# Performance work log

Hardware: AMD Instinct MI355X
Metric: run time of the kernel (lower is better)

Reference implementation:

```python
import jax, jax.numpy as jnp
import numpy as np

N_NODES = 50000
N_EDGES = 800000
IN_FEATS = 128
H_FEATS = 32
HEADS = 4
OUT_FEATS = 32
OUT_HEADS = 1
NEG_SLOPE = 0.2


def setup_inputs() -> dict:
    key = jax.random.key(0)
    ks = jax.random.split(key, 20)
    s = 0.05
    return {
        "features": jax.random.normal(ks[0], (N_NODES, IN_FEATS), jnp.float32),
        "src": jax.random.randint(ks[1], (N_EDGES,), 0, N_NODES, jnp.int32),
        "dst": jax.random.randint(ks[2], (N_EDGES,), 0, N_NODES, jnp.int32),
        "Ws0": jax.random.normal(ks[3], (IN_FEATS, HEADS * H_FEATS), jnp.float32) * s,
        "bs0": jnp.zeros((HEADS * H_FEATS,), jnp.float32),
        "Wd0": jax.random.normal(ks[4], (IN_FEATS, HEADS * H_FEATS), jnp.float32) * s,
        "bd0": jnp.zeros((HEADS * H_FEATS,), jnp.float32),
        "a0": jax.random.normal(ks[5], (HEADS, H_FEATS), jnp.float32) * s,
        "Ws1": jax.random.normal(ks[6], (HEADS * H_FEATS, HEADS * H_FEATS), jnp.float32) * s,
        "bs1": jnp.zeros((HEADS * H_FEATS,), jnp.float32),
        "Wd1": jax.random.normal(ks[7], (HEADS * H_FEATS, HEADS * H_FEATS), jnp.float32) * s,
        "bd1": jnp.zeros((HEADS * H_FEATS,), jnp.float32),
        "a1": jax.random.normal(ks[8], (HEADS, H_FEATS), jnp.float32) * s,
        "Ws2": jax.random.normal(ks[9], (HEADS * H_FEATS, OUT_HEADS * OUT_FEATS), jnp.float32) * s,
        "bs2": jnp.zeros((OUT_HEADS * OUT_FEATS,), jnp.float32),
        "Wd2": jax.random.normal(ks[10], (HEADS * H_FEATS, OUT_HEADS * OUT_FEATS), jnp.float32) * s,
        "bd2": jnp.zeros((OUT_HEADS * OUT_FEATS,), jnp.float32),
        "a2": jax.random.normal(ks[11], (OUT_HEADS, OUT_FEATS), jnp.float32) * s,
    }


def gatv2_conv(x, src, dst, Ws, bs, Wd, bd, attn, n_nodes):
    """DGL GATv2Conv (share_weights=False, residual=False, no dropout)."""
    heads, f = attn.shape
    feat_src = (x @ Ws + bs).reshape(-1, heads, f)  # [N, H, F]
    feat_dst = (x @ Wd + bd).reshape(-1, heads, f)  # [N, H, F]
    # per-edge GATv2 score: LeakyReLU(Wsrc h_u + Wdst h_v) . a
    e = jax.nn.leaky_relu(feat_src[src] + feat_dst[dst], NEG_SLOPE)  # [E, H, F]
    logits = jnp.einsum("ehf,hf->eh", e, attn)  # [E, H]
    # edge softmax over incoming edges of each dst node
    m = jax.ops.segment_max(logits, dst, num_segments=n_nodes)  # [N, H]
    ex = jnp.exp(logits - m[dst])
    denom = jax.ops.segment_sum(ex, dst, num_segments=n_nodes)  # [N, H]
    alpha = ex / denom[dst]  # [E, H]
    # scatter-aggregate messages
    msg = feat_src[src] * alpha[..., None]  # [E, H, F]
    return jax.ops.segment_sum(msg, dst, num_segments=n_nodes)  # [N, H, F]


def reference(features, src, dst,
              Ws0, bs0, Wd0, bd0, a0,
              Ws1, bs1, Wd1, bd1, a1,
              Ws2, bs2, Wd2, bd2, a2):
    n = features.shape[0]
    h = gatv2_conv(features, src, dst, Ws0, bs0, Wd0, bd0, a0, n)
    h = jax.nn.relu(h.reshape(n, -1))
    h = gatv2_conv(h, src, dst, Ws1, bs1, Wd1, bd1, a1, n)
    h = jax.nn.relu(h.reshape(n, -1))
    h = gatv2_conv(h, src, dst, Ws2, bs2, Wd2, bd2, a2, n)
    return h.mean(axis=1)  # [N, OUT_FEATS]
```

## Files before the change

kernel.cpp:

```cpp
#include <hip/hip_runtime.h>

typedef __attribute__((ext_vector_type(8))) short bf16x8;
typedef __attribute__((ext_vector_type(4))) float f32x4;

#define LOG2E 1.4426950408889634f

#define BINSH 8
#define NBIN 196
#define CHUNK 4096
#define K4CAP 6144

__device__ __forceinline__ unsigned bf_rn(float f) {
    unsigned u = __float_as_uint(f);
    u += 0x7fffu + ((u >> 16) & 1u);
    return u >> 16;
}
__device__ __forceinline__ float bf_lo(unsigned u) { return __uint_as_float(u << 16); }
__device__ __forceinline__ float bf_hi(unsigned u) { return __uint_as_float(u & 0xffff0000u); }

template <int CTRL>
__device__ __forceinline__ float dpp_radd(float x) {
    int t = __builtin_amdgcn_update_dpp(0, __float_as_int(x), CTRL, 0xF, 0xF, true);
    return x + __int_as_float(t);
}
__device__ __forceinline__ float sum8(float p) {
    p = dpp_radd<0x141>(p);
    p = dpp_radd<0x1B>(p);
    p = dpp_radd<0xB1>(p);
    return p;
}
__device__ __forceinline__ float sum4(float p) {
    p = dpp_radd<0xB1>(p);
    p = dpp_radd<0x4E>(p);
    return p;
}
__device__ __forceinline__ float dpp_swap1(float x) {
    return __int_as_float(__builtin_amdgcn_update_dpp(0, __float_as_int(x), 0xB1, 0xF, 0xF, true));
}

__device__ __forceinline__ float fast_exp2(float x) {
#if __has_builtin(__builtin_amdgcn_exp2f)
    return __builtin_amdgcn_exp2f(x);
#else
    return __expf(x * 0.6931471805599453f);
#endif
}


__global__ __launch_bounds__(256) void bin_count(const int* __restrict__ dst,
                                                 int* __restrict__ binCnt, int e) {
    __shared__ int hist[NBIN];
    for (int t = threadIdx.x; t < NBIN; t += 256) hist[t] = 0;
    __syncthreads();
    int base = blockIdx.x * CHUNK;
    int cnt = min(CHUNK, e - base);
    for (int j = threadIdx.x; j < cnt; j += 256)
        atomicAdd(&hist[dst[base + j] >> BINSH], 1);
    __syncthreads();
    for (int t = threadIdx.x; t < NBIN; t += 256)
        if (hist[t]) atomicAdd(&binCnt[t], hist[t]);
}

__global__ void bin_scan(const int* __restrict__ binCnt, int* __restrict__ binBase,
                         int* __restrict__ binCur, int* __restrict__ rowp, int n, int e) {
    int t = threadIdx.x;
    int v = (t < NBIN) ? binCnt[t] : 0;
    int lane = t & 63, w = t >> 6;
    int incl = v;
    for (int off = 1; off < 64; off <<= 1) {
        int tt = __shfl_up(incl, off);
        if (lane >= off) incl += tt;
    }
    __shared__ int wsum[4];
    if (lane == 63) wsum[w] = incl;
    __syncthreads();
    int wpre = 0;
    for (int i = 0; i < w; ++i) wpre += wsum[i];
    int excl = wpre + incl - v;
    if (t < NBIN) { binBase[t] = excl; binCur[t] = excl; }
    if (t == 0) { binBase[NBIN] = e; rowp[n] = e; }
}

__global__ __launch_bounds__(256) void bin_scatter(
    const int* __restrict__ src, const int* __restrict__ dst,
    int* __restrict__ binCur, unsigned* __restrict__ ebin, int e) {
    __shared__ int hist[256];
    __shared__ int seg[256];
    __shared__ int gbase[NBIN];
    __shared__ unsigned pack[CHUNK];
    for (int t = threadIdx.x; t < 256; t += 256) hist[t] = 0;
    __syncthreads();
    int base = blockIdx.x * CHUNK;
    int cnt = min(CHUNK, e - base);

    for (int j = threadIdx.x; j < cnt; j += 256)
        atomicAdd(&hist[dst[base + j] >> BINSH], 1);
    __syncthreads();
    if (threadIdx.x < 64) {
        int l = threadIdx.x;
        int s = 0, loc[4];
#pragma unroll
        for (int k = 0; k < 4; ++k) { loc[k] = s; s += hist[l * 4 + k]; }
        int incl = s;
        for (int off = 1; off < 64; off <<= 1) {
            int tt = __shfl_up(incl, off);
            if (l >= off) incl += tt;
        }
        int excl = incl - s;
#pragma unroll
        for (int k = 0; k < 4; ++k) seg[l * 4 + k] = excl + loc[k];
    }
    __syncthreads();
    if (threadIdx.x < NBIN && hist[threadIdx.x])
        gbase[threadIdx.x] = atomicAdd(&binCur[threadIdx.x], hist[threadIdx.x]);
    __syncthreads();
    for (int t = threadIdx.x; t < 256; t += 256) hist[t] = seg[t];
    __syncthreads();
    for (int j = threadIdx.x; j < cnt; j += 256) {
        int d = dst[base + j], s = src[base + j];
        int b = d >> BINSH, dl = d & ((1 << BINSH) - 1);
        int pos = atomicAdd(&hist[b], 1);
        pack[pos] = ((unsigned)b << 24) | ((unsigned)dl << 16) | (unsigned)s;
    }
    __syncthreads();
    for (int j = threadIdx.x; j < cnt; j += 256) {
        unsigned wv = pack[j];
        int b = wv >> 24;
        ebin[gbase[b] + (j - seg[b])] = wv;
    }
}

__global__ __launch_bounds__(256) void csr_build(
    const unsigned* __restrict__ ebin, const int* __restrict__ binBase,
    int* __restrict__ rowp, int* __restrict__ csrc, int n) {
    __shared__ int hist[256];
    __shared__ int seg[256];
    __shared__ unsigned stage[K4CAP];
    int b = blockIdx.x;
    int e0 = binBase[b], e1 = binBase[b + 1];
    int n0 = b << BINSH;
    int nn = min(256, n - n0);
    for (int t = threadIdx.x; t < 256; t += 256) hist[t] = 0;
    __syncthreads();
    for (int i = e0 + threadIdx.x; i < e1; i += 256) {
        unsigned wv = ebin[i];
        atomicAdd(&hist[(wv >> 16) & 255], 1);
        int off = i - e0;
        if (off < K4CAP) stage[off] = wv;
    }
    __syncthreads();
    if (threadIdx.x < 64) {
        int l = threadIdx.x;
        int s = 0, loc[4];
#pragma unroll
        for (int k = 0; k < 4; ++k) { loc[k] = s; s += hist[l * 4 + k]; }
        int incl = s;
        for (int off = 1; off < 64; off <<= 1) {
            int tt = __shfl_up(incl, off);
            if (l >= off) incl += tt;
        }
        int excl = incl - s;
#pragma unroll
        for (int k = 0; k < 4; ++k) seg[l * 4 + k] = excl + loc[k];
    }
    __syncthreads();
    for (int t = threadIdx.x; t < nn; t += 256) rowp[n0 + t] = e0 + seg[t];
    for (int t = threadIdx.x; t < 256; t += 256) hist[t] = seg[t];
    __syncthreads();
    for (int i = e0 + threadIdx.x; i < e1; i += 256) {
        int off = i - e0;
        unsigned wv = (off < K4CAP) ? stage[off] : ebin[i];
        int dl = (wv >> 16) & 255;
        int pos = e0 + atomicAdd(&hist[dl], 1);
        csrc[pos] = (int)(wv & 0xFFFFu);
    }
}


__global__ __launch_bounds__(256) void prep(
    const float* __restrict__ x, unsigned short* __restrict__ xb, int n4,
    const float* __restrict__ Ws0, const float* __restrict__ Wd0,
    const float* __restrict__ Ws1, const float* __restrict__ Wd1,
    const float* __restrict__ Ws2, const float* __restrict__ Wd2,
    unsigned short* __restrict__ wt0, unsigned short* __restrict__ wt1,
    unsigned short* __restrict__ wt2, int* __restrict__ binCnt) {
    int gid = blockIdx.x * blockDim.x + threadIdx.x;
    if (gid < NBIN) binCnt[gid] = 0;
    if (gid < n4) {
        float4 v = *(const float4*)(x + (size_t)gid * 4);
        ushort4 r;
        r.x = (unsigned short)bf_rn(v.x); r.y = (unsigned short)bf_rn(v.y);
        r.z = (unsigned short)bf_rn(v.z); r.w = (unsigned short)bf_rn(v.w);
        *(ushort4*)(xb + (size_t)gid * 4) = r;
    } else {
        int g = gid - n4;
        if (g < 65536) {
            int l = g >> 15, loc = g & 32767;
            int c = loc >> 7, k = loc & 127;
            const float* W = (c < 128) ? (l ? Ws1 : Ws0) : (l ? Wd1 : Wd0);
            int cc = c & 127;
            float v = W[(size_t)k * 128 + cc];
            (l ? wt1 : wt0)[loc] = (unsigned short)bf_rn(v);
        } else if (g < 65536 + 8192) {
            int loc = g - 65536;
            int c = loc >> 7, k = loc & 127;
            const float* W = (c < 32) ? Ws2 : Wd2;
            int cc = (c < 32) ? c : c - 32;
            float v = W[(size_t)k * 32 + cc];
            wt2[loc] = (unsigned short)bf_rn(v);
        }
    }
}


template <int COLS2>
__global__ __launch_bounds__(256) void gemm_dual2(
    const unsigned short* __restrict__ xb, const unsigned short* __restrict__ wt,
    const float* __restrict__ bs, const float* __restrict__ bd,
    unsigned short* __restrict__ fs, unsigned short* __restrict__ fd,
    int n, int nch) {
    constexpr int C  = COLS2 / 2;
    constexpr int NC = COLS2 / 64;

    const int lane = threadIdx.x & 63;
    const int m = lane & 15, quad = lane >> 4;
    const int gwid = blockIdx.x * 4 + (threadIdx.x >> 6);
    const int nwaves = gridDim.x * 4;
    const int cs = gwid % NC;
    const int cstride = nwaves / NC;

    float biasv[4];
#pragma unroll
    for (int ct = 0; ct < 4; ++ct) {
        int col = cs * 64 + ct * 16 + m;
        biasv[ct] = (col < C) ? bs[col] : bd[col - C];
    }

    for (int chunk = gwid / NC; chunk < nch; chunk += cstride) {
        const size_t r0 = (size_t)chunk * 64;

        f32x4 acc[4][4];
#pragma unroll
        for (int rt = 0; rt < 4; ++rt)
#pragma unroll
            for (int ct = 0; ct < 4; ++ct) acc[rt][ct] = (f32x4){0.f, 0.f, 0.f, 0.f};

#pragma unroll
        for (int ks = 0; ks < 4; ++ks) {
            const int ko = ks * 32 + quad * 8;
            bf16x8 a[4], b[4];
#pragma unroll
            for (int rt = 0; rt < 4; ++rt)
                a[rt] = *(const bf16x8*)(xb + (r0 + rt * 16 + m) * 128 + ko);
#pragma unroll
            for (int ct = 0; ct < 4; ++ct)
                b[ct] = *(const bf16x8*)(wt + (size_t)(cs * 64 + ct * 16 + m) * 128 + ko);
#pragma unroll
            for (int rt = 0; rt < 4; ++rt)
#pragma unroll
                for (int ct = 0; ct < 4; ++ct)
                    acc[rt][ct] = __builtin_amdgcn_mfma_f32_16x16x32_bf16(a[rt], b[ct], acc[rt][ct], 0, 0, 0);
        }

        const int odd = m & 1;
#pragma unroll
        for (int ct = 0; ct < 4; ++ct) {
            int colE = cs * 64 + ct * 16 + (m & ~1);
            unsigned short* ptr = (colE < C) ? fs : fd;
            int cc = (colE < C) ? colE : colE - C;
#pragma unroll
            for (int rt = 0; rt < 4; ++rt) {
                float v0 = acc[rt][ct][0] + biasv[ct];
                float v1 = acc[rt][ct][1] + biasv[ct];
                float v2 = acc[rt][ct][2] + biasv[ct];
                float v3 = acc[rt][ct][3] + biasv[ct];
                float s0 = dpp_swap1(v0), s1 = dpp_swap1(v1);
                float s2 = dpp_swap1(v2), s3 = dpp_swap1(v3);
                float aLo = odd ? s2 : v0, aHi = odd ? v2 : s0;
                float bLo = odd ? s3 : v1, bHi = odd ? v3 : s1;
                int rowA = (int)r0 + rt * 16 + quad * 4 + (odd ? 2 : 0);
                unsigned pa = (bf_rn(aHi) << 16) | bf_rn(aLo);
                unsigned pb = (bf_rn(bHi) << 16) | bf_rn(bLo);
                if (rowA < n)     *(unsigned*)(ptr + (size_t)rowA * C + cc)       = pa;
                if (rowA + 1 < n) *(unsigned*)(ptr + ((size_t)rowA + 1) * C + cc) = pb;
            }
        }
    }
}


#define EDGE_BODY(u, mval)                                          \
    do {                                                            \
        float x0 = bf_lo((u).x), x1 = bf_hi((u).x);                 \
        float x2 = bf_lo((u).y), x3 = bf_hi((u).y);                 \
        float t0 = x0 + fd0, t1 = x1 + fd1;                         \
        float t2 = x2 + fd2, t3 = x3 + fd3;                         \
        float p = a060 * t0;                                        \
        p = fmaf(a040, fabsf(t0), p);                               \
        p = fmaf(a061, t1, p); p = fmaf(a041, fabsf(t1), p);        \
        p = fmaf(a062, t2, p); p = fmaf(a042, fabsf(t2), p);        \
        p = fmaf(a063, t3, p); p = fmaf(a043, fabsf(t3), p);        \
        p = sum8(p);                                                \
        float ex = fast_exp2(p) * (mval);                           \
        denom += ex;                                                \
        acc0 = fmaf(ex, x0, acc0); acc1 = fmaf(ex, x1, acc1);       \
        acc2 = fmaf(ex, x2, acc2); acc3 = fmaf(ex, x3, acc3);       \
    } while (0)

#define EB8(u, mval)                                                \
    do {                                                            \
        float x0 = bf_lo((u).x), x1 = bf_hi((u).x);                 \
        float x2 = bf_lo((u).y), x3 = bf_hi((u).y);                 \
        float x4 = bf_lo((u).z), x5 = bf_hi((u).z);                 \
        float x6 = bf_lo((u).w), x7 = bf_hi((u).w);                 \
        float t0 = x0 + fd0, t1 = x1 + fd1;                         \
        float t2 = x2 + fd2, t3 = x3 + fd3;                         \
        float t4 = x4 + fd4, t5 = x5 + fd5;                         \
        float t6 = x6 + fd6, t7 = x7 + fd7;                         \
        float p0 = a60_0 * t0;                                      \
        p0 = fmaf(a40_0, fabsf(t0), p0);                            \
        p0 = fmaf(a60_1, t1, p0); p0 = fmaf(a40_1, fabsf(t1), p0);  \
        p0 = fmaf(a60_2, t2, p0); p0 = fmaf(a40_2, fabsf(t2), p0);  \
        p0 = fmaf(a60_3, t3, p0); p0 = fmaf(a40_3, fabsf(t3), p0);  \
        float p1 = a60_4 * t4;                                      \
        p1 = fmaf(a40_4, fabsf(t4), p1);                            \
        p1 = fmaf(a60_5, t5, p1); p1 = fmaf(a40_5, fabsf(t5), p1);  \
        p1 = fmaf(a60_6, t6, p1); p1 = fmaf(a40_6, fabsf(t6), p1);  \
        p1 = fmaf(a60_7, t7, p1); p1 = fmaf(a40_7, fabsf(t7), p1);  \
        float p = sum4(p0 + p1);                                    \
        float ex = fast_exp2(p) * (mval);                           \
        denom += ex;                                                \
        acc0 = fmaf(ex, x0, acc0); acc1 = fmaf(ex, x1, acc1);       \
        acc2 = fmaf(ex, x2, acc2); acc3 = fmaf(ex, x3, acc3);       \
        acc4 = fmaf(ex, x4, acc4); acc5 = fmaf(ex, x5, acc5);       \
        acc6 = fmaf(ex, x6, acc6); acc7 = fmaf(ex, x7, acc7);       \
    } while (0)

__global__ __launch_bounds__(256) void conv128(
    const unsigned short* __restrict__ fs, const unsigned short* __restrict__ fd,
    const float* __restrict__ attn, const int* __restrict__ rowp,
    const int* __restrict__ csrc, unsigned short* __restrict__ out, int n) {
    const int nwaves = gridDim.x * 4;
    const int wid = blockIdx.x * 4 + (threadIdx.x >> 6);
    const int lane = threadIdx.x & 63;
    const int slot = lane >> 4;
    const int c = lane & 15;

    float4 av0 = *(const float4*)(attn + c * 8);
    float4 av1 = *(const float4*)(attn + c * 8 + 4);
    const float a60_0 = av0.x * 0.6f * LOG2E, a40_0 = av0.x * 0.4f * LOG2E;
    const float a60_1 = av0.y * 0.6f * LOG2E, a40_1 = av0.y * 0.4f * LOG2E;
    const float a60_2 = av0.z * 0.6f * LOG2E, a40_2 = av0.z * 0.4f * LOG2E;
    const float a60_3 = av0.w * 0.6f * LOG2E, a40_3 = av0.w * 0.4f * LOG2E;
    const float a60_4 = av1.x * 0.6f * LOG2E, a40_4 = av1.x * 0.4f * LOG2E;
    const float a60_5 = av1.y * 0.6f * LOG2E, a40_5 = av1.y * 0.4f * LOG2E;
    const float a60_6 = av1.z * 0.6f * LOG2E, a40_6 = av1.z * 0.4f * LOG2E;
    const float a60_7 = av1.w * 0.6f * LOG2E, a40_7 = av1.w * 0.4f * LOG2E;

    const int q = n / nwaves, r = n % nwaves;
    const int row0 = wid * q + min(wid, r);
    const int row1 = row0 + q + (wid < r ? 1 : 0);

    const unsigned short* fsc = fs + c * 8;

    for (int row = row0; row < row1; ++row) {
        uint4 ud = *(const uint4*)(fd + (size_t)row * 128 + c * 8);
        float fd0 = bf_lo(ud.x), fd1 = bf_hi(ud.x);
        float fd2 = bf_lo(ud.y), fd3 = bf_hi(ud.y);
        float fd4 = bf_lo(ud.z), fd5 = bf_hi(ud.z);
        float fd6 = bf_lo(ud.w), fd7 = bf_hi(ud.w);
        int rs = rowp[row], re = rowp[row + 1];
        float acc0 = 0.f, acc1 = 0.f, acc2 = 0.f, acc3 = 0.f;
        float acc4 = 0.f, acc5 = 0.f, acc6 = 0.f, acc7 = 0.f, denom = 0.f;

        int i = rs;
        const int ng = (re - rs) >> 3;
        if (ng > 0) {
            int ib = rs + 2 * slot;
            int sA0 = csrc[ib], sA1 = csrc[ib + 1];
            uint4 uA0 = *(const uint4*)(fsc + ((size_t)sA0 << 7));
            uint4 uA1 = *(const uint4*)(fsc + ((size_t)sA1 << 7));
            for (int g2 = 1; g2 < ng; ++g2) {
                ib += 8;
                int sB0 = csrc[ib], sB1 = csrc[ib + 1];
                uint4 uB0 = *(const uint4*)(fsc + ((size_t)sB0 << 7));
                uint4 uB1 = *(const uint4*)(fsc + ((size_t)sB1 << 7));
                EB8(uA0, 1.0f);
                EB8(uA1, 1.0f);
                uA0 = uB0; uA1 = uB1;
            }
            EB8(uA0, 1.0f);
            EB8(uA1, 1.0f);
            i = rs + ng * 8;
        }
        for (; i + 3 < re; i += 4) {
            int s = csrc[i + slot];
            uint4 u = *(const uint4*)(fsc + ((size_t)s << 7));
            EB8(u, 1.0f);
        }
        if (i < re) {
            int idx = i + slot;
            int s = csrc[min(idx, re - 1)];
            uint4 u = *(const uint4*)(fsc + ((size_t)s << 7));
            float mval = (idx < re) ? 1.f : 0.f;
            EB8(u, mval);
        }
        acc0 += __shfl_xor(acc0, 16); acc1 += __shfl_xor(acc1, 16);
        acc2 += __shfl_xor(acc2, 16); acc3 += __shfl_xor(acc3, 16);
        acc4 += __shfl_xor(acc4, 16); acc5 += __shfl_xor(acc5, 16);
        acc6 += __shfl_xor(acc6, 16); acc7 += __shfl_xor(acc7, 16);
        denom += __shfl_xor(denom, 16);
        acc0 += __shfl_xor(acc0, 32); acc1 += __shfl_xor(acc1, 32);
        acc2 += __shfl_xor(acc2, 32); acc3 += __shfl_xor(acc3, 32);
        acc4 += __shfl_xor(acc4, 32); acc5 += __shfl_xor(acc5, 32);
        acc6 += __shfl_xor(acc6, 32); acc7 += __shfl_xor(acc7, 32);
        denom += __shfl_xor(denom, 32);
        float inv = (re > rs) ? 1.f / denom : 0.f;
        float r0 = fmaxf(acc0 * inv, 0.f), r1 = fmaxf(acc1 * inv, 0.f);
        float r2 = fmaxf(acc2 * inv, 0.f), r3 = fmaxf(acc3 * inv, 0.f);
        float r4 = fmaxf(acc4 * inv, 0.f), r5 = fmaxf(acc5 * inv, 0.f);
        float r6 = fmaxf(acc6 * inv, 0.f), r7 = fmaxf(acc7 * inv, 0.f);
        if (slot == 0) {
            uint4 o;
            o.x = (bf_rn(r1) << 16) | bf_rn(r0);
            o.y = (bf_rn(r3) << 16) | bf_rn(r2);
            o.z = (bf_rn(r5) << 16) | bf_rn(r4);
            o.w = (bf_rn(r7) << 16) | bf_rn(r6);
            *(uint4*)(out + (size_t)row * 128 + c * 8) = o;
        }
    }
}

__global__ __launch_bounds__(256) void conv32(
    const unsigned short* __restrict__ fs, const unsigned short* __restrict__ fd,
    const float* __restrict__ attn, const int* __restrict__ rowp,
    const int* __restrict__ csrc, float* __restrict__ out, int n) {
    const int nwaves = gridDim.x * 4;
    const int wid = blockIdx.x * 4 + (threadIdx.x >> 6);
    const int lane = threadIdx.x & 63;
    const int g = lane >> 3;
    const int c = lane & 7;

    float4 av = *(const float4*)(attn + c * 4);
    const float a060 = av.x * 0.6f * LOG2E, a040 = av.x * 0.4f * LOG2E;
    const float a061 = av.y * 0.6f * LOG2E, a041 = av.y * 0.4f * LOG2E;
    const float a062 = av.z * 0.6f * LOG2E, a042 = av.z * 0.4f * LOG2E;
    const float a063 = av.w * 0.6f * LOG2E, a043 = av.w * 0.4f * LOG2E;

    const int q = n / nwaves, r = n % nwaves;
    const int row0 = wid * q + min(wid, r);
    const int row1 = row0 + q + (wid < r ? 1 : 0);

    const unsigned short* fsc = fs + c * 4;

    for (int row = row0; row < row1; ++row) {
        uint2 ud = *(const uint2*)(fd + (size_t)row * 32 + c * 4);
        float fd0 = bf_lo(ud.x), fd1 = bf_hi(ud.x);
        float fd2 = bf_lo(ud.y), fd3 = bf_hi(ud.y);
        int rs = rowp[row], re = rowp[row + 1];
        float acc0 = 0.f, acc1 = 0.f, acc2 = 0.f, acc3 = 0.f, denom = 0.f;

        int i = rs;
        for (; i + 15 < re; i += 16) {
            int s0 = csrc[i + g];
            int s1 = csrc[i + 8 + g];
            uint2 u0 = *(const uint2*)(fsc + ((size_t)s0 << 5));
            uint2 u1 = *(const uint2*)(fsc + ((size_t)s1 << 5));
            EDGE_BODY(u0, 1.0f);
            EDGE_BODY(u1, 1.0f);
        }
        for (; i + 7 < re; i += 8) {
            int s = csrc[i + g];
            uint2 u = *(const uint2*)(fsc + ((size_t)s << 5));
            EDGE_BODY(u, 1.0f);
        }
        if (i < re) {
            int idx = i + g;
            int s = csrc[min(idx, re - 1)];
            uint2 u = *(const uint2*)(fsc + ((size_t)s << 5));
            float mval = (idx < re) ? 1.f : 0.f;
            EDGE_BODY(u, mval);
        }
        acc0 = dpp_radd<0x128>(acc0); acc1 = dpp_radd<0x128>(acc1);
        acc2 = dpp_radd<0x128>(acc2); acc3 = dpp_radd<0x128>(acc3);
        denom = dpp_radd<0x128>(denom);
        acc0 += __shfl_xor(acc0, 16); acc1 += __shfl_xor(acc1, 16);
        acc2 += __shfl_xor(acc2, 16); acc3 += __shfl_xor(acc3, 16);
        denom += __shfl_xor(denom, 16);
        acc0 += __shfl_xor(acc0, 32); acc1 += __shfl_xor(acc1, 32);
        acc2 += __shfl_xor(acc2, 32); acc3 += __shfl_xor(acc3, 32);
        denom += __shfl_xor(denom, 32);
        float inv = (re > rs) ? 1.f / denom : 0.f;
        if (lane < 8) {
            float4 o;
            o.x = acc0 * inv; o.y = acc1 * inv;
            o.z = acc2 * inv; o.w = acc3 * inv;
            *(float4*)(out + (size_t)row * 32 + c * 4) = o;
        }
    }
}


extern "C" void kernel_launch(void* const* d_in, const int* in_sizes, int n_in,
                              void* d_out, int out_size, void* d_ws, size_t ws_size,
                              hipStream_t stream) {
    const float* feats = (const float*)d_in[0];
    const int*   src   = (const int*)d_in[1];
    const int*   dst   = (const int*)d_in[2];
    const float* Ws0 = (const float*)d_in[3],  *bs0 = (const float*)d_in[4];
    const float* Wd0 = (const float*)d_in[5],  *bd0 = (const float*)d_in[6];
    const float* a0  = (const float*)d_in[7];
    const float* Ws1 = (const float*)d_in[8],  *bs1 = (const float*)d_in[9];
    const float* Wd1 = (const float*)d_in[10], *bd1 = (const float*)d_in[11];
    const float* a1  = (const float*)d_in[12];
    const float* Ws2 = (const float*)d_in[13], *bs2 = (const float*)d_in[14];
    const float* Wd2 = (const float*)d_in[15], *bd2 = (const float*)d_in[16];
    const float* a2  = (const float*)d_in[17];

    const int N = in_sizes[0] / 128;
    const int E = in_sizes[1];
    const int nch = (N + 63) / 64;
    const int NPAD = nch * 64;

    char* ws = (char*)d_ws;
    const size_t featB = (size_t)NPAD * 128 * 2;
    unsigned short* xb  = (unsigned short*)(ws);
    unsigned short* hb  = (unsigned short*)(ws + featB);
    unsigned short* fsb = (unsigned short*)(ws + 2 * featB);
    unsigned short* fdb = (unsigned short*)(ws + 3 * featB);
    char* p = ws + 4 * featB;
    unsigned short* wt0 = (unsigned short*)p; p += 256 * 128 * 2;
    unsigned short* wt1 = (unsigned short*)p; p += 256 * 128 * 2;
    unsigned short* wt2 = (unsigned short*)p; p += 64 * 128 * 2;
    int* rowp    = (int*)p;      p += ((size_t)(N + 1) * 4 + 255) / 256 * 256;
    int* binCnt  = (int*)p;      p += (NBIN * 4 + 255) / 256 * 256;
    int* binBase = (int*)p;      p += ((NBIN + 1) * 4 + 255) / 256 * 256;
    int* binCur  = (int*)p;      p += (NBIN * 4 + 255) / 256 * 256;
    unsigned* ebin = (unsigned*)p; p += (size_t)E * 4;
    int* csrc    = (int*)p;

    const int nchunks = (E + CHUNK - 1) / CHUNK;
    const int n4 = N * 128 / 4;

    prep<<<(n4 + 73728 + 255) / 256, 256, 0, stream>>>(
        feats, xb, n4, Ws0, Wd0, Ws1, Wd1, Ws2, Wd2, wt0, wt1, wt2, binCnt);

    bin_count<<<nchunks, 256, 0, stream>>>(dst, binCnt, E);
    bin_scan<<<1, 256, 0, stream>>>(binCnt, binBase, binCur, rowp, N, E);
    bin_scatter<<<nchunks, 256, 0, stream>>>(src, dst, binCur, ebin, E);
    csr_build<<<NBIN, 256, 0, stream>>>(ebin, binBase, rowp, csrc, N);

    const int g256 = nch;
    const int g64  = (nch + 3) / 4;
    const int convGrid = 2048;

    gemm_dual2<256><<<g256, 256, 0, stream>>>(xb, wt0, bs0, bd0, fsb, fdb, N, nch);
    conv128<<<convGrid, 256, 0, stream>>>(fsb, fdb, a0, rowp, csrc, hb, N);
    gemm_dual2<256><<<g256, 256, 0, stream>>>(hb, wt1, bs1, bd1, fsb, fdb, N, nch);
    conv128<<<convGrid, 256, 0, stream>>>(fsb, fdb, a1, rowp, csrc, hb, N);
    gemm_dual2<64><<<g64, 256, 0, stream>>>(hb, wt2, bs2, bd2, fsb, fdb, N, nch);
    conv32<<<convGrid, 256, 0, stream>>>(fsb, fdb, a2, rowp, csrc, (float*)d_out, N);
}
```

Before: 303.2 us.

## Use atomic work-stealing row chunks in GAT conv kernels and widen edge unroll

Replaces the static per-wave row partition in conv128 and conv32 with dynamic chunks of 8 rows fetched through a global atomic counter, zeroed in the prep kernel. This aims to balance load across waves when node in-degrees vary. conv128's edge loop also drops the software-pipelined 8-edge prefetch in favour of a 16-edge unrolled batch of gathers. The change adds one atomic per chunk and loses the explicit cross-iteration prefetch.

```diff
diff --git a/kernel.cpp b/kernel.cpp
--- a/kernel.cpp
+++ b/kernel.cpp
@@ -9,6 +9,7 @@
 #define NBIN 196
 #define CHUNK 4096
 #define K4CAP 6144
+#define RPC 8
 
 __device__ __forceinline__ unsigned bf_rn(float f) {
     unsigned u = __float_as_uint(f);
@@ -183,9 +184,11 @@
     const float* __restrict__ Ws1, const float* __restrict__ Wd1,
     const float* __restrict__ Ws2, const float* __restrict__ Wd2,
     unsigned short* __restrict__ wt0, unsigned short* __restrict__ wt1,
-    unsigned short* __restrict__ wt2, int* __restrict__ binCnt) {
+    unsigned short* __restrict__ wt2, int* __restrict__ binCnt,
+    int* __restrict__ wkctr) {
     int gid = blockIdx.x * blockDim.x + threadIdx.x;
     if (gid < NBIN) binCnt[gid] = 0;
+    if (gid < 8) wkctr[gid] = 0;
     if (gid < n4) {
         float4 v = *(const float4*)(x + (size_t)gid * 4);
         ushort4 r;
@@ -339,9 +342,8 @@
 __global__ __launch_bounds__(256) void conv128(
     const unsigned short* __restrict__ fs, const unsigned short* __restrict__ fd,
     const float* __restrict__ attn, const int* __restrict__ rowp,
-    const int* __restrict__ csrc, unsigned short* __restrict__ out, int n) {
-    const int nwaves = gridDim.x * 4;
-    const int wid = blockIdx.x * 4 + (threadIdx.x >> 6);
+    const int* __restrict__ csrc, unsigned short* __restrict__ out, int n,
+    int* __restrict__ wkctr) {
     const int lane = threadIdx.x & 63;
     const int slot = lane >> 4;
     const int c = lane & 15;
@@ -357,76 +359,84 @@
     const float a60_6 = av1.z * 0.6f * LOG2E, a40_6 = av1.z * 0.4f * LOG2E;
     const float a60_7 = av1.w * 0.6f * LOG2E, a40_7 = av1.w * 0.4f * LOG2E;
 
-    const int q = n / nwaves, r = n % nwaves;
-    const int row0 = wid * q + min(wid, r);
-    const int row1 = row0 + q + (wid < r ? 1 : 0);
-
     const unsigned short* fsc = fs + c * 8;
 
-    for (int row = row0; row < row1; ++row) {
-        uint4 ud = *(const uint4*)(fd + (size_t)row * 128 + c * 8);
-        float fd0 = bf_lo(ud.x), fd1 = bf_hi(ud.x);
-        float fd2 = bf_lo(ud.y), fd3 = bf_hi(ud.y);
-        float fd4 = bf_lo(ud.z), fd5 = bf_hi(ud.z);
-        float fd6 = bf_lo(ud.w), fd7 = bf_hi(ud.w);
-        int rs = rowp[row], re = rowp[row + 1];
-        float acc0 = 0.f, acc1 = 0.f, acc2 = 0.f, acc3 = 0.f;
-        float acc4 = 0.f, acc5 = 0.f, acc6 = 0.f, acc7 = 0.f, denom = 0.f;
-
-        int i = rs;
-        const int ng = (re - rs) >> 3;
-        if (ng > 0) {
-            int ib = rs + 2 * slot;
-            int sA0 = csrc[ib], sA1 = csrc[ib + 1];
-            uint4 uA0 = *(const uint4*)(fsc + ((size_t)sA0 << 7));
-            uint4 uA1 = *(const uint4*)(fsc + ((size_t)sA1 << 7));
-            for (int g2 = 1; g2 < ng; ++g2) {
-                ib += 8;
-                int sB0 = csrc[ib], sB1 = csrc[ib + 1];
-                uint4 uB0 = *(const uint4*)(fsc + ((size_t)sB0 << 7));
-                uint4 uB1 = *(const uint4*)(fsc + ((size_t)sB1 << 7));
-                EB8(uA0, 1.0f);
-                EB8(uA1, 1.0f);
-                uA0 = uB0; uA1 = uB1;
-            }
-            EB8(uA0, 1.0f);
-            EB8(uA1, 1.0f);
-            i = rs + ng * 8;
-        }
-        for (; i + 3 < re; i += 4) {
-            int s = csrc[i + slot];
-            uint4 u = *(const uint4*)(fsc + ((size_t)s << 7));
-            EB8(u, 1.0f);
-        }
-        if (i < re) {
-            int idx = i + slot;
-            int s = csrc[min(idx, re - 1)];
-            uint4 u = *(const uint4*)(fsc + ((size_t)s << 7));
-            float mval = (idx < re) ? 1.f : 0.f;
-            EB8(u, mval);
-        }
-        acc0 += __shfl_xor(acc0, 16); acc1 += __shfl_xor(acc1, 16);
-        acc2 += __shfl_xor(acc2, 16); acc3 += __shfl_xor(acc3, 16);
-        acc4 += __shfl_xor(acc4, 16); acc5 += __shfl_xor(acc5, 16);
-        acc6 += __shfl_xor(acc6, 16); acc7 += __shfl_xor(acc7, 16);
-        denom += __shfl_xor(denom, 16);
-        acc0 += __shfl_xor(acc0, 32); acc1 += __shfl_xor(acc1, 32);
-        acc2 += __shfl_xor(acc2, 32); acc3 += __shfl_xor(acc3, 32);
-        acc4 += __shfl_xor(acc4, 32); acc5 += __shfl_xor(acc5, 32);
-        acc6 += __shfl_xor(acc6, 32); acc7 += __shfl_xor(acc7, 32);
-        denom += __shfl_xor(denom, 32);
-        float inv = (re > rs) ? 1.f / denom : 0.f;
-        float r0 = fmaxf(acc0 * inv, 0.f), r1 = fmaxf(acc1 * inv, 0.f);
-        float r2 = fmaxf(acc2 * inv, 0.f), r3 = fmaxf(acc3 * inv, 0.f);
-        float r4 = fmaxf(acc4 * inv, 0.f), r5 = fmaxf(acc5 * inv, 0.f);
-        float r6 = fmaxf(acc6 * inv, 0.f), r7 = fmaxf(acc7 * inv, 0.f);
-        if (slot == 0) {
-            uint4 o;
-            o.x = (bf_rn(r1) << 16) | bf_rn(r0);
-            o.y = (bf_rn(r3) << 16) | bf_rn(r2);
-            o.z = (bf_rn(r5) << 16) | bf_rn(r4);
-            o.w = (bf_rn(r7) << 16) | bf_rn(r6);
-            *(uint4*)(out + (size_t)row * 128 + c * 8) = o;
+    for (;;) {
+        int ch;
+        if (lane == 0) ch = atomicAdd(wkctr, 1);
+        ch = __shfl(ch, 0);
+        const int row0 = ch * RPC;
+        if (row0 >= n) break;
+        const int rowE = min(row0 + RPC, n);
+
+        for (int row = row0; row < rowE; ++row) {
+            uint4 ud = *(const uint4*)(fd + (size_t)row * 128 + c * 8);
+            float fd0 = bf_lo(ud.x), fd1 = bf_hi(ud.x);
+            float fd2 = bf_lo(ud.y), fd3 = bf_hi(ud.y);
+            float fd4 = bf_lo(ud.z), fd5 = bf_hi(ud.z);
+            float fd6 = bf_lo(ud.w), fd7 = bf_hi(ud.w);
+            int rs = rowp[row], re = rowp[row + 1];
+            float acc0 = 0.f, acc1 = 0.f, acc2 = 0.f, acc3 = 0.f;
+            float acc4 = 0.f, acc5 = 0.f, acc6 = 0.f, acc7 = 0.f, denom = 0.f;
+
+            int i = rs;
+            for (; i + 15 < re; i += 16) {
+                int s0 = csrc[i + slot];
+                int s1 = csrc[i + 4 + slot];
+                int s2 = csrc[i + 8 + slot];
+                int s3 = csrc[i + 12 + slot];
+                uint4 u0 = *(const uint4*)(fsc + ((size_t)s0 << 7));
+                uint4 u1 = *(const uint4*)(fsc + ((size_t)s1 << 7));
+                uint4 u2 = *(const uint4*)(fsc + ((size_t)s2 << 7));
+                uint4 u3 = *(const uint4*)(fsc + ((size_t)s3 << 7));
+                EB8(u0, 1.0f);
+                EB8(u1, 1.0f);
+                EB8(u2, 1.0f);
+                EB8(u3, 1.0f);
+            }
+            for (; i + 7 < re; i += 8) {
+                int s0 = csrc[i + slot];
+                int s1 = csrc[i + 4 + slot];
+                uint4 u0 = *(const uint4*)(fsc + ((size_t)s0 << 7));
+                uint4 u1 = *(const uint4*)(fsc + ((size_t)s1 << 7));
+                EB8(u0, 1.0f);
+                EB8(u1, 1.0f);
+            }
+            for (; i + 3 < re; i += 4) {
+                int s = csrc[i + slot];
+                uint4 u = *(const uint4*)(fsc + ((size_t)s << 7));
+                EB8(u, 1.0f);
+            }
+            if (i < re) {
+                int idx = i + slot;
+                int s = csrc[min(idx, re - 1)];
+                uint4 u = *(const uint4*)(fsc + ((size_t)s << 7));
+                float mval = (idx < re) ? 1.f : 0.f;
+                EB8(u, mval);
+            }
+            acc0 += __shfl_xor(acc0, 16); acc1 += __shfl_xor(acc1, 16);
+            acc2 += __shfl_xor(acc2, 16); acc3 += __shfl_xor(acc3, 16);
+            acc4 += __shfl_xor(acc4, 16); acc5 += __shfl_xor(acc5, 16);
+            acc6 += __shfl_xor(acc6, 16); acc7 += __shfl_xor(acc7, 16);
+            denom += __shfl_xor(denom, 16);
+            acc0 += __shfl_xor(acc0, 32); acc1 += __shfl_xor(acc1, 32);
+            acc2 += __shfl_xor(acc2, 32); acc3 += __shfl_xor(acc3, 32);
+            acc4 += __shfl_xor(acc4, 32); acc5 += __shfl_xor(acc5, 32);
+            acc6 += __shfl_xor(acc6, 32); acc7 += __shfl_xor(acc7, 32);
+            denom += __shfl_xor(denom, 32);
+            float inv = (re > rs) ? 1.f / denom : 0.f;
+            float r0 = fmaxf(acc0 * inv, 0.f), r1 = fmaxf(acc1 * inv, 0.f);
+            float r2 = fmaxf(acc2 * inv, 0.f), r3 = fmaxf(acc3 * inv, 0.f);
+            float r4 = fmaxf(acc4 * inv, 0.f), r5 = fmaxf(acc5 * inv, 0.f);
+            float r6 = fmaxf(acc6 * inv, 0.f), r7 = fmaxf(acc7 * inv, 0.f);
+            if (slot == 0) {
+                uint4 o;
+                o.x = (bf_rn(r1) << 16) | bf_rn(r0);
+                o.y = (bf_rn(r3) << 16) | bf_rn(r2);
+                o.z = (bf_rn(r5) << 16) | bf_rn(r4);
+                o.w = (bf_rn(r7) << 16) | bf_rn(r6);
+                *(uint4*)(out + (size_t)row * 128 + c * 8) = o;
+            }
         }
     }
 }
@@ -434,9 +444,8 @@
 __global__ __launch_bounds__(256) void conv32(
     const unsigned short* __restrict__ fs, const unsigned short* __restrict__ fd,
     const float* __restrict__ attn, const int* __restrict__ rowp,
-    const int* __restrict__ csrc, float* __restrict__ out, int n) {
-    const int nwaves = gridDim.x * 4;
-    const int wid = blockIdx.x * 4 + (threadIdx.x >> 6);
+    const int* __restrict__ csrc, float* __restrict__ out, int n,
+    int* __restrict__ wkctr) {
     const int lane = threadIdx.x & 63;
     const int g = lane >> 3;
     const int c = lane & 7;
@@ -447,55 +456,60 @@
     const float a062 = av.z * 0.6f * LOG2E, a042 = av.z * 0.4f * LOG2E;
     const float a063 = av.w * 0.6f * LOG2E, a043 = av.w * 0.4f * LOG2E;
 
-    const int q = n / nwaves, r = n % nwaves;
-    const int row0 = wid * q + min(wid, r);
-    const int row1 = row0 + q + (wid < r ? 1 : 0);
-
     const unsigned short* fsc = fs + c * 4;
 
-    for (int row = row0; row < row1; ++row) {
-        uint2 ud = *(const uint2*)(fd + (size_t)row * 32 + c * 4);
-        float fd0 = bf_lo(ud.x), fd1 = bf_hi(ud.x);
-        float fd2 = bf_lo(ud.y), fd3 = bf_hi(ud.y);
-        int rs = rowp[row], re = rowp[row + 1];
-        float acc0 = 0.f, acc1 = 0.f, acc2 = 0.f, acc3 = 0.f, denom = 0.f;
-
-        int i = rs;
-        for (; i + 15 < re; i += 16) {
-            int s0 = csrc[i + g];
-            int s1 = csrc[i + 8 + g];
-            uint2 u0 = *(const uint2*)(fsc + ((size_t)s0 << 5));
-            uint2 u1 = *(const uint2*)(fsc + ((size_t)s1 << 5));
-            EDGE_BODY(u0, 1.0f);
-            EDGE_BODY(u1, 1.0f);
-        }
-        for (; i + 7 < re; i += 8) {
-            int s = csrc[i + g];
-            uint2 u = *(const uint2*)(fsc + ((size_t)s << 5));
-            EDGE_BODY(u, 1.0f);
-        }
-        if (i < re) {
-            int idx = i + g;
-            int s = csrc[min(idx, re - 1)];
-            uint2 u = *(const uint2*)(fsc + ((size_t)s << 5));
-            float mval = (idx < re) ? 1.f : 0.f;
-            EDGE_BODY(u, mval);
-        }
-        acc0 = dpp_radd<0x128>(acc0); acc1 = dpp_radd<0x128>(acc1);
-        acc2 = dpp_radd<0x128>(acc2); acc3 = dpp_radd<0x128>(acc3);
-        denom = dpp_radd<0x128>(denom);
-        acc0 += __shfl_xor(acc0, 16); acc1 += __shfl_xor(acc1, 16);
-        acc2 += __shfl_xor(acc2, 16); acc3 += __shfl_xor(acc3, 16);
-        denom += __shfl_xor(denom, 16);
-        acc0 += __shfl_xor(acc0, 32); acc1 += __shfl_xor(acc1, 32);
-        acc2 += __shfl_xor(acc2, 32); acc3 += __shfl_xor(acc3, 32);
-        denom += __shfl_xor(denom, 32);
-        float inv = (re > rs) ? 1.f / denom : 0.f;
-        if (lane < 8) {
-            float4 o;
-            o.x = acc0 * inv; o.y = acc1 * inv;
-            o.z = acc2 * inv; o.w = acc3 * inv;
-            *(float4*)(out + (size_t)row * 32 + c * 4) = o;
+    for (;;) {
+        int ch;
+        if (lane == 0) ch = atomicAdd(wkctr, 1);
+        ch = __shfl(ch, 0);
+        const int row0 = ch * RPC;
+        if (row0 >= n) break;
+        const int rowE = min(row0 + RPC, n);
+
+        for (int row = row0; row < rowE; ++row) {
+            uint2 ud = *(const uint2*)(fd + (size_t)row * 32 + c * 4);
+            float fd0 = bf_lo(ud.x), fd1 = bf_hi(ud.x);
+            float fd2 = bf_lo(ud.y), fd3 = bf_hi(ud.y);
+            int rs = rowp[row], re = rowp[row + 1];
+            float acc0 = 0.f, acc1 = 0.f, acc2 = 0.f, acc3 = 0.f, denom = 0.f;
+
+            int i = rs;
+            for (; i + 15 < re; i += 16) {
+                int s0 = csrc[i + g];
+                int s1 = csrc[i + 8 + g];
+                uint2 u0 = *(const uint2*)(fsc + ((size_t)s0 << 5));
+                uint2 u1 = *(const uint2*)(fsc + ((size_t)s1 << 5));
+                EDGE_BODY(u0, 1.0f);
+                EDGE_BODY(u1, 1.0f);
+            }
+            for (; i + 7 < re; i += 8) {
+                int s = csrc[i + g];
+                uint2 u = *(const uint2*)(fsc + ((size_t)s << 5));
+                EDGE_BODY(u, 1.0f);
+            }
+            if (i < re) {
+                int idx = i + g;
+                int s = csrc[min(idx, re - 1)];
+                uint2 u = *(const uint2*)(fsc + ((size_t)s << 5));
+                float mval = (idx < re) ? 1.f : 0.f;
+                EDGE_BODY(u, mval);
+            }
+            acc0 = dpp_radd<0x128>(acc0); acc1 = dpp_radd<0x128>(acc1);
+            acc2 = dpp_radd<0x128>(acc2); acc3 = dpp_radd<0x128>(acc3);
+            denom = dpp_radd<0x128>(denom);
+            acc0 += __shfl_xor(acc0, 16); acc1 += __shfl_xor(acc1, 16);
+            acc2 += __shfl_xor(acc2, 16); acc3 += __shfl_xor(acc3, 16);
+            denom += __shfl_xor(denom, 16);
+            acc0 += __shfl_xor(acc0, 32); acc1 += __shfl_xor(acc1, 32);
+            acc2 += __shfl_xor(acc2, 32); acc3 += __shfl_xor(acc3, 32);
+            denom += __shfl_xor(denom, 32);
+            float inv = (re > rs) ? 1.f / denom : 0.f;
+            if (lane < 8) {
+                float4 o;
+                o.x = acc0 * inv; o.y = acc1 * inv;
+                o.z = acc2 * inv; o.w = acc3 * inv;
+                *(float4*)(out + (size_t)row * 32 + c * 4) = o;
+            }
         }
     }
 }
@@ -536,6 +550,7 @@
     int* binCnt  = (int*)p;      p += (NBIN * 4 + 255) / 256 * 256;
     int* binBase = (int*)p;      p += ((NBIN + 1) * 4 + 255) / 256 * 256;
     int* binCur  = (int*)p;      p += (NBIN * 4 + 255) / 256 * 256;
+    int* wkctr   = (int*)p;      p += 256;
     unsigned* ebin = (unsigned*)p; p += (size_t)E * 4;
     int* csrc    = (int*)p;
 
@@ -543,7 +558,7 @@
     const int n4 = N * 128 / 4;
 
     prep<<<(n4 + 73728 + 255) / 256, 256, 0, stream>>>(
-        feats, xb, n4, Ws0, Wd0, Ws1, Wd1, Ws2, Wd2, wt0, wt1, wt2, binCnt);
+        feats, xb, n4, Ws0, Wd0, Ws1, Wd1, Ws2, Wd2, wt0, wt1, wt2, binCnt, wkctr);
 
     bin_count<<<nchunks, 256, 0, stream>>>(dst, binCnt, E);
     bin_scan<<<1, 256, 0, stream>>>(binCnt, binBase, binCur, rowp, N, E);
@@ -555,9 +570,9 @@
     const int convGrid = 2048;
 
     gemm_dual2<256><<<g256, 256, 0, stream>>>(xb, wt0, bs0, bd0, fsb, fdb, N, nch);
-    conv128<<<convGrid, 256, 0, stream>>>(fsb, fdb, a0, rowp, csrc, hb, N);
+    conv128<<<convGrid, 256, 0, stream>>>(fsb, fdb, a0, rowp, csrc, hb, N, &wkctr[0]);
     gemm_dual2<256><<<g256, 256, 0, stream>>>(hb, wt1, bs1, bd1, fsb, fdb, N, nch);
-    conv128<<<convGrid, 256, 0, stream>>>(fsb, fdb, a1, rowp, csrc, hb, N);
+    conv128<<<convGrid, 256, 0, stream>>>(fsb, fdb, a1, rowp, csrc, hb, N, &wkctr[1]);
     gemm_dual2<64><<<g64, 256, 0, stream>>>(hb, wt2, bs2, bd2, fsb, fdb, N, nch);
-    conv32<<<convGrid, 256, 0, stream>>>(fsb, fdb, a2, rowp, csrc, (float*)d_out, N);
-}
+    conv32<<<convGrid, 256, 0, stream>>>(fsb, fdb, a2, rowp, csrc, (float*)d_out, N, &wkctr[2]);
+}
```

Measured after the change: 739.7 us. 144% more time.
